# Kernel optimization log

Hardware: AMD Instinct MI355X
Metric: run time of the kernel (lower is better)

The kernel has to match this reference:

```python
import jax, jax.numpy as jnp
import numpy as np

M, K, O = 8192, 4096, 4096
WORDS = K // 32
INT32_MAX = 2147483647


def _unpack_ternary(nz, sgn):
    """Unpack bit-packed ternary weights.
    nz, sgn: [O, WORDS] int32 bitmasks. Bit j of word w corresponds to input
    column w*32 + j. weight = 0 if nz bit clear, else +1 (sgn bit clear) or -1.
    Returns dense float32 [O, K].
    """
    shifts = jnp.arange(32, dtype=jnp.uint32)
    nzb = (nz.astype(jnp.uint32)[:, :, None] >> shifts) & jnp.uint32(1)   # [O, WORDS, 32]
    sgb = (sgn.astype(jnp.uint32)[:, :, None] >> shifts) & jnp.uint32(1)  # [O, WORDS, 32]
    w = nzb.astype(jnp.float32) * (1.0 - 2.0 * sgb.astype(jnp.float32))
    return w.reshape(nz.shape[0], -1)  # [O, K]


def setup_inputs() -> dict:
    key = jax.random.key(0)
    k1, k2, k3, k4, k5 = jax.random.split(key, 5)
    x = jax.random.normal(k1, (M, K), dtype=jnp.float32)
    nz = jax.random.randint(k2, (O, WORDS), 0, INT32_MAX, dtype=jnp.int32)
    sgn = jax.random.randint(k3, (O, WORDS), 0, INT32_MAX, dtype=jnp.int32)
    bias = jax.random.normal(k4, (O,), dtype=jnp.float32) * 0.01
    alpha = jax.random.uniform(k5, (O,), dtype=jnp.float32, minval=0.5, maxval=1.5)
    return {"x": x, "nz": nz, "sgn": sgn, "bias": bias, "alpha": alpha}


def reference(x, nz, sgn, bias, alpha):
    # y = (x @ W^T) * alpha + bias, W dequantized from ternary bit-packs
    W = _unpack_ternary(nz, sgn)                       # [O, K]
    y = jnp.einsum('mk,ok->mo', x, W)                  # [M, O]
    y = y * alpha[None, :] + bias[None, :]
    return y
```

## Files before the change

kernel.cpp:

```cpp
#include <hip/hip_runtime.h>
#include <stdint.h>

#define M_DIM 8192
#define K_DIM 4096
#define O_DIM 4096
#define NWORDS 128

typedef __attribute__((ext_vector_type(8))) short bf16x8;
typedef __attribute__((ext_vector_type(4))) float f32x4;
typedef __attribute__((ext_vector_type(4))) float fvec4;
typedef __attribute__((ext_vector_type(4))) unsigned uvec4;

__device__ __forceinline__ unsigned f32_to_bf16u(float f) {
  union { float f; unsigned u; } v; v.f = f;
  return (v.u + 0x7FFFu + ((v.u >> 16) & 1u)) >> 16;
}

__device__ __forceinline__ unsigned pack_bf16x2(float lo, float hi) {
  return f32_to_bf16u(lo) | (f32_to_bf16u(hi) << 16);
}

__global__ __launch_bounds__(256) void prep_kernel(const fvec4* __restrict__ x,
                                                   uvec4* __restrict__ xb4,
                                                   const unsigned* __restrict__ nz,
                                                   const unsigned* __restrict__ sgn,
                                                   unsigned short* __restrict__ wb) {
  const int b   = blockIdx.x;
  const int tid = threadIdx.x;
  if (b < 2048) {
    for (long p = (long)b * 256 + tid; p < 4194304; p += 524288) {
      const fvec4 v0 = x[2 * p];
      const fvec4 v1 = x[2 * p + 1];
      uvec4 o;
      o.x = pack_bf16x2(v0.x, v0.y);
      o.y = pack_bf16x2(v0.z, v0.w);
      o.z = pack_bf16x2(v1.x, v1.y);
      o.w = pack_bf16x2(v1.z, v1.w);
      xb4[p] = o;
    }
  } else {
    for (long i = (long)(b - 2048) * 256 + tid; i < 2097152; i += 131072) {
      const int w = (int)(i >> 2);
      const int q = (int)(i & 3);
      const unsigned n = nz[w] >> (8 * q);
      const unsigned s = sgn[w] >> (8 * q);
      unsigned out[4];
#pragma unroll
      for (int pq = 0; pq < 4; ++pq) {
        const int j0 = 2 * pq, j1 = 2 * pq + 1;
        unsigned lo = ((n >> j0) & 1u) ? (0x3F80u | (((s >> j0) & 1u) << 15)) : 0u;
        unsigned hi = ((n >> j1) & 1u) ? (0x3F80u | (((s >> j1) & 1u) << 15)) : 0u;
        out[pq] = lo | (hi << 16);
      }
      uvec4 v = { out[0], out[1], out[2], out[3] };
      *(uvec4*)(wb + (long)w * 32 + q * 8) = v;
    }
  }
}

__global__ __launch_bounds__(512, 2) void gemm_kernel(const unsigned short* __restrict__ A,
                                                      const unsigned short* __restrict__ B,
                                                      const float* __restrict__ bias,
                                                      const float* __restrict__ alpha,
                                                      float* __restrict__ C) {
  __shared__ unsigned short lds[65536];

  const int tid  = threadIdx.x;
  const int lane = tid & 63;
  const int wave = tid >> 6;
  const int wm   = wave >> 2;
  const int wn   = wave & 3;

  const int wg   = blockIdx.x;
  const int swz  = (wg & 7) * 64 + (wg >> 3);
  const int nBlk = (swz & 15) * 256;
  const int mBlk = (swz >> 4) * 256;

  const unsigned short* Apan = A + (long)mBlk * K_DIM;
  const unsigned short* Bpan = B + (long)nBlk * K_DIM;

  int lOff[2], gOff[2];
#pragma unroll
  for (int l = 0; l < 2; ++l) {
    const int o = (l * 512 + tid) * 16;
    const int r = o >> 7;
    const int q = ((o >> 4) & 7) ^ (r & 7);
    lOff[l] = o;
    gOff[l] = r * K_DIM + q * 8;
  }

  const int fr  = lane & 15;
  const int fq  = lane >> 4;
  const int sl0 = fq ^ (fr & 7);
  const int aFB = fr * 64;
  const int bFB = (wn & 1) * 4096 + fr * 64;
  const int A0S = wm * 8192;
  const int A1S = (2 + wm) * 8192;
  const int B0S = 32768 + (wn >> 1) * 8192;
  const int B1S = 32768 + (2 + (wn >> 1)) * 8192;

  f32x4  acc[8][4] = {};
  bf16x8 a[2][2], bv[4][2];

#define STAGE(SUBv, BUFv, TILEv) do {                                          \
    const unsigned short* s_ = (((SUBv) < 2) ? Apan : Bpan)                    \
        + (long)((SUBv) & 1) * (128 * K_DIM) + (long)(TILEv) * 64;             \
    const int dB = ((((SUBv) < 2) ? 0 : 32768)                                 \
        + (((BUFv) * 2) + ((SUBv) & 1)) * 8192) * 2;                           \
    __builtin_amdgcn_global_load_lds(                                          \
        (const __attribute__((address_space(1))) void*)(s_ + gOff[0]),         \
        (__attribute__((address_space(3))) void*)((char*)lds + dB + lOff[0]),  \
        16, 0, 0);                                                             \
    __builtin_amdgcn_global_load_lds(                                          \
        (const __attribute__((address_space(1))) void*)(s_ + gOff[1]),         \
        (__attribute__((address_space(3))) void*)((char*)lds + dB + lOff[1]),  \
        16, 0, 0);                                                             \
  } while (0)

#define LOADA2(BASE, P)                                                        \
  _Pragma("unroll")                                                            \
  for (int i = 0; i < 2; ++i) {                                                \
    const int off_ = (BASE) + ((P) * 2 + i) * 1024 + aFB;                      \
    a[i][0] = *(const bf16x8*)(lds + off_ + sl0 * 8);                          \
    a[i][1] = *(const bf16x8*)(lds + off_ + (sl0 ^ 4) * 8);                    \
  }

#define LOADB(BASE)                                                            \
  _Pragma("unroll")                                                            \
  for (int j = 0; j < 4; ++j) {                                                \
    const int off_ = (BASE) + bFB + j * 1024;                                  \
    bv[j][0] = *(const bf16x8*)(lds + off_ + sl0 * 8);                         \
    bv[j][1] = *(const bf16x8*)(lds + off_ + (sl0 ^ 4) * 8);                   \
  }

#define MFMA2(P)                                                               \
  _Pragma("unroll")                                                            \
  for (int kh = 0; kh < 2; ++kh)                                               \
    _Pragma("unroll")                                                          \
    for (int i = 0; i < 2; ++i)                                                \
      _Pragma("unroll")                                                        \
      for (int tn = 0; tn < 4; ++tn)                                           \
        acc[(P) * 2 + i][tn] = __builtin_amdgcn_mfma_f32_16x16x32_bf16(        \
            a[i][kh], bv[tn][kh], acc[(P) * 2 + i][tn], 0, 0, 0);

#define PRE12()   asm volatile("s_waitcnt lgkmcnt(8)" ::: "memory")
#define MID()  __builtin_amdgcn_s_barrier();                                   \
               asm volatile("s_waitcnt lgkmcnt(0)" ::: "memory");              \
               __builtin_amdgcn_s_setprio(1)
#define ENDPH()   __builtin_amdgcn_s_setprio(0); __builtin_amdgcn_s_barrier()
#define ENDVM4()  __builtin_amdgcn_s_setprio(0);                               \
                  asm volatile("s_waitcnt vmcnt(4)" ::: "memory");             \
                  __builtin_amdgcn_s_barrier()
#define ENDVM0()  __builtin_amdgcn_s_setprio(0);                               \
                  asm volatile("s_waitcnt vmcnt(0)" ::: "memory");             \
                  __builtin_amdgcn_s_barrier()

  STAGE(2, 0, 0); STAGE(3, 0, 0); STAGE(0, 0, 0); STAGE(1, 0, 0);
  STAGE(2, 1, 1); STAGE(3, 1, 1);
  asm volatile("s_waitcnt vmcnt(4)" ::: "memory");
  __builtin_amdgcn_s_barrier();

  for (int it = 0; it < (K_DIM / 64) / 2 - 1; ++it) {
    const int t1 = 2 * it + 1, t2 = 2 * it + 2, t3 = 2 * it + 3;
    LOADA2(A0S, 0); LOADB(B0S); STAGE(1, 1, t1); PRE12();
                                                 MID(); MFMA2(0); ENDPH();
    LOADA2(A0S, 1);             STAGE(0, 1, t1); MID(); MFMA2(1); ENDPH();
    LOADA2(A0S, 2);             STAGE(2, 0, t2); MID(); MFMA2(2); ENDPH();
    LOADA2(A0S, 3);             STAGE(3, 0, t2); MID(); MFMA2(3); ENDVM4();
    LOADA2(A1S, 0); LOADB(B1S); STAGE(0, 0, t2); PRE12();
                                                 MID(); MFMA2(0); ENDPH();
    LOADA2(A1S, 1);             STAGE(1, 0, t2); MID(); MFMA2(1); ENDPH();
    LOADA2(A1S, 2);             STAGE(2, 1, t3); MID(); MFMA2(2); ENDPH();
    LOADA2(A1S, 3);             STAGE(3, 1, t3); MID(); MFMA2(3); ENDVM4();
  }

  LOADA2(A0S, 0); LOADB(B0S); STAGE(1, 1, 63); PRE12();
                                               MID(); MFMA2(0); ENDPH();
  LOADA2(A0S, 1);             STAGE(0, 1, 63); MID(); MFMA2(1); ENDPH();
  LOADA2(A0S, 2);                              MID(); MFMA2(2); ENDPH();
  LOADA2(A0S, 3);                              MID(); MFMA2(3); ENDVM0();
  LOADA2(A1S, 0); LOADB(B1S);                  MID(); MFMA2(0); ENDPH();
  LOADA2(A1S, 1);                              MID(); MFMA2(1); ENDPH();
  LOADA2(A1S, 2);                              MID(); MFMA2(2); ENDPH();
  LOADA2(A1S, 3);                              MID(); MFMA2(3);
  __builtin_amdgcn_s_setprio(0);

#pragma unroll
  for (int tn = 0; tn < 4; ++tn) {
    const int n = nBlk + wn * 64 + tn * 16 + fr;
    const float al = alpha[n];
    const float bi = bias[n];
#pragma unroll
    for (int tm = 0; tm < 8; ++tm) {
      const int mBase = mBlk + wm * 128 + tm * 16 + fq * 4;
#pragma unroll
      for (int r = 0; r < 4; ++r)
        __builtin_nontemporal_store(acc[tm][tn][r] * al + bi,
                                    C + (long)(mBase + r) * O_DIM + n);
    }
  }

#undef STAGE
#undef LOADA2
#undef LOADB
#undef MFMA2
#undef PRE12
#undef MID
#undef ENDPH
#undef ENDVM4
#undef ENDVM0
}

__global__ __launch_bounds__(256) void fallback_kernel(const float* __restrict__ x,
                                                       const unsigned* __restrict__ nz,
                                                       const unsigned* __restrict__ sgn,
                                                       const float* __restrict__ bias,
                                                       const float* __restrict__ alpha,
                                                       float* __restrict__ y) {
  long gid = (long)blockIdx.x * 256 + threadIdx.x;
  int o = (int)(gid % O_DIM);
  long m = gid / O_DIM;
  const float* xr = x + m * K_DIM;
  float s = 0.f;
  for (int w = 0; w < NWORDS; ++w) {
    unsigned n = nz[o * NWORDS + w];
    unsigned g = sgn[o * NWORDS + w];
    for (int j = 0; j < 32; ++j) {
      if ((n >> j) & 1u) {
        float v = xr[w * 32 + j];
        s += ((g >> j) & 1u) ? -v : v;
      }
    }
  }
  y[gid] = s * alpha[o] + bias[o];
}

extern "C" void kernel_launch(void* const* d_in, const int* in_sizes, int n_in,
                              void* d_out, int out_size, void* d_ws, size_t ws_size,
                              hipStream_t stream) {
  const float*    x     = (const float*)d_in[0];
  const unsigned* nz    = (const unsigned*)d_in[1];
  const unsigned* sgn   = (const unsigned*)d_in[2];
  const float*    bias  = (const float*)d_in[3];
  const float*    alpha = (const float*)d_in[4];
  float*          y     = (float*)d_out;

  const size_t xb_bytes = (size_t)M_DIM * K_DIM * 2;
  const size_t wb_bytes = (size_t)O_DIM * K_DIM * 2;

  if (ws_size >= xb_bytes + wb_bytes) {
    unsigned short* xb = (unsigned short*)d_ws;
    unsigned short* wb = (unsigned short*)((char*)d_ws + xb_bytes);

    prep_kernel<<<2560, 256, 0, stream>>>((const fvec4*)x, (uvec4*)xb, nz, sgn, wb);
    gemm_kernel<<<512, 512, 0, stream>>>(xb, wb, bias, alpha, y);
  } else {
    fallback_kernel<<<(long)M_DIM * O_DIM / 256, 256, 0, stream>>>(x, nz, sgn, bias, alpha, y);
  }
}
```

Before: 435.3 us.

## Switch GEMM inner loop from 16x16x32 to 32x32x16 bf16 MFMA tiles

Replaces the 16x16x32 bf16 MFMA fragments with 32x32x16 MFMA, changing each wave's accumulator layout to 4x2 tiles of 32x32, and reworks LDS fragment loads and the epilogue store mapping to match. Larger MFMA tiles cut the LDS reads per FLOP and the MFMA instruction count. In exchange the LDS access pattern under the existing XOR swizzle changes, which may cause bank conflicts. The output index mapping must match the 32x32 accumulator layout exactly.

After: 456.6 us. +4.9%, slower.

```diff
diff --git a/kernel.cpp b/kernel.cpp
--- a/kernel.cpp
+++ b/kernel.cpp
@@ -7,7 +7,7 @@
 #define NWORDS 128
 
 typedef __attribute__((ext_vector_type(8))) short bf16x8;
-typedef __attribute__((ext_vector_type(4))) float f32x4;
+typedef __attribute__((ext_vector_type(16))) float f32x16;
 typedef __attribute__((ext_vector_type(4))) float fvec4;
 typedef __attribute__((ext_vector_type(4))) unsigned uvec4;
 
@@ -89,18 +89,21 @@
     gOff[l] = r * K_DIM + q * 8;
   }
 
-  const int fr  = lane & 15;
-  const int fq  = lane >> 4;
-  const int sl0 = fq ^ (fr & 7);
-  const int aFB = fr * 64;
-  const int bFB = (wn & 1) * 4096 + fr * 64;
+  const int rl = lane & 31;
+  const int hi = lane >> 5;
+  const int x7 = lane & 7;
+  int qs[4];
+#pragma unroll
+  for (int g = 0; g < 4; ++g) qs[g] = (2 * g + hi) ^ x7;
+  const int aRB = rl * 64;
+  const int bNB = (wn & 1) * 4096 + rl * 64;
   const int A0S = wm * 8192;
   const int A1S = (2 + wm) * 8192;
   const int B0S = 32768 + (wn >> 1) * 8192;
   const int B1S = 32768 + (2 + (wn >> 1)) * 8192;
 
-  f32x4  acc[8][4] = {};
-  bf16x8 a[2][2], bv[4][2];
+  f32x16 acc[4][2] = {};
+  bf16x8 a[4], bv[2][4];
 
 #define STAGE(SUBv, BUFv, TILEv) do {                                          \
     const unsigned short* s_ = (((SUBv) < 2) ? Apan : Bpan)                    \
@@ -117,31 +120,25 @@
         16, 0, 0);                                                             \
   } while (0)
 
-#define LOADA2(BASE, P)                                                        \
+#define LOADA32(BASE, MB)                                                      \
   _Pragma("unroll")                                                            \
-  for (int i = 0; i < 2; ++i) {                                                \
-    const int off_ = (BASE) + ((P) * 2 + i) * 1024 + aFB;                      \
-    a[i][0] = *(const bf16x8*)(lds + off_ + sl0 * 8);                          \
-    a[i][1] = *(const bf16x8*)(lds + off_ + (sl0 ^ 4) * 8);                    \
-  }
-
-#define LOADB(BASE)                                                            \
+  for (int g = 0; g < 4; ++g)                                                  \
+    a[g] = *(const bf16x8*)(lds + (BASE) + (MB) * 2048 + aRB + qs[g] * 8);
+
+#define LOADB32(BASE)                                                          \
   _Pragma("unroll")                                                            \
-  for (int j = 0; j < 4; ++j) {                                                \
-    const int off_ = (BASE) + bFB + j * 1024;                                  \
-    bv[j][0] = *(const bf16x8*)(lds + off_ + sl0 * 8);                         \
-    bv[j][1] = *(const bf16x8*)(lds + off_ + (sl0 ^ 4) * 8);                   \
-  }
-
-#define MFMA2(P)                                                               \
+  for (int nt = 0; nt < 2; ++nt)                                               \
+    _Pragma("unroll")                                                          \
+    for (int g = 0; g < 4; ++g)                                                \
+      bv[nt][g] = *(const bf16x8*)(lds + (BASE) + bNB + nt * 2048 + qs[g] * 8);
+
+#define MFMAPH(MB)                                                             \
   _Pragma("unroll")                                                            \
-  for (int kh = 0; kh < 2; ++kh)                                               \
+  for (int g = 0; g < 4; ++g)                                                  \
     _Pragma("unroll")                                                          \
-    for (int i = 0; i < 2; ++i)                                                \
-      _Pragma("unroll")                                                        \
-      for (int tn = 0; tn < 4; ++tn)                                           \
-        acc[(P) * 2 + i][tn] = __builtin_amdgcn_mfma_f32_16x16x32_bf16(        \
-            a[i][kh], bv[tn][kh], acc[(P) * 2 + i][tn], 0, 0, 0);
+    for (int nt = 0; nt < 2; ++nt)                                             \
+      acc[MB][nt] = __builtin_amdgcn_mfma_f32_32x32x16_bf16(                   \
+          a[g], bv[nt][g], acc[MB][nt], 0, 0, 0);
 
 #define PRE12()   asm volatile("s_waitcnt lgkmcnt(8)" ::: "memory")
 #define MID()  __builtin_amdgcn_s_barrier();                                   \
@@ -162,48 +159,51 @@
 
   for (int it = 0; it < (K_DIM / 64) / 2 - 1; ++it) {
     const int t1 = 2 * it + 1, t2 = 2 * it + 2, t3 = 2 * it + 3;
-    LOADA2(A0S, 0); LOADB(B0S); STAGE(1, 1, t1); PRE12();
-                                                 MID(); MFMA2(0); ENDPH();
-    LOADA2(A0S, 1);             STAGE(0, 1, t1); MID(); MFMA2(1); ENDPH();
-    LOADA2(A0S, 2);             STAGE(2, 0, t2); MID(); MFMA2(2); ENDPH();
-    LOADA2(A0S, 3);             STAGE(3, 0, t2); MID(); MFMA2(3); ENDVM4();
-    LOADA2(A1S, 0); LOADB(B1S); STAGE(0, 0, t2); PRE12();
-                                                 MID(); MFMA2(0); ENDPH();
-    LOADA2(A1S, 1);             STAGE(1, 0, t2); MID(); MFMA2(1); ENDPH();
-    LOADA2(A1S, 2);             STAGE(2, 1, t3); MID(); MFMA2(2); ENDPH();
-    LOADA2(A1S, 3);             STAGE(3, 1, t3); MID(); MFMA2(3); ENDVM4();
-  }
-
-  LOADA2(A0S, 0); LOADB(B0S); STAGE(1, 1, 63); PRE12();
-                                               MID(); MFMA2(0); ENDPH();
-  LOADA2(A0S, 1);             STAGE(0, 1, 63); MID(); MFMA2(1); ENDPH();
-  LOADA2(A0S, 2);                              MID(); MFMA2(2); ENDPH();
-  LOADA2(A0S, 3);                              MID(); MFMA2(3); ENDVM0();
-  LOADA2(A1S, 0); LOADB(B1S);                  MID(); MFMA2(0); ENDPH();
-  LOADA2(A1S, 1);                              MID(); MFMA2(1); ENDPH();
-  LOADA2(A1S, 2);                              MID(); MFMA2(2); ENDPH();
-  LOADA2(A1S, 3);                              MID(); MFMA2(3);
+    LOADA32(A0S, 0); LOADB32(B0S); STAGE(1, 1, t1); PRE12();
+                                                    MID(); MFMAPH(0); ENDPH();
+    LOADA32(A0S, 1);               STAGE(0, 1, t1); MID(); MFMAPH(1); ENDPH();
+    LOADA32(A0S, 2);               STAGE(2, 0, t2); MID(); MFMAPH(2); ENDPH();
+    LOADA32(A0S, 3);               STAGE(3, 0, t2); MID(); MFMAPH(3); ENDVM4();
+    LOADA32(A1S, 0); LOADB32(B1S); STAGE(0, 0, t2); PRE12();
+                                                    MID(); MFMAPH(0); ENDPH();
+    LOADA32(A1S, 1);               STAGE(1, 0, t2); MID(); MFMAPH(1); ENDPH();
+    LOADA32(A1S, 2);               STAGE(2, 1, t3); MID(); MFMAPH(2); ENDPH();
+    LOADA32(A1S, 3);               STAGE(3, 1, t3); MID(); MFMAPH(3); ENDVM4();
+  }
+
+  LOADA32(A0S, 0); LOADB32(B0S); STAGE(1, 1, 63); PRE12();
+                                                  MID(); MFMAPH(0); ENDPH();
+  LOADA32(A0S, 1);               STAGE(0, 1, 63); MID(); MFMAPH(1); ENDPH();
+  LOADA32(A0S, 2);                                MID(); MFMAPH(2); ENDPH();
+  LOADA32(A0S, 3);                                MID(); MFMAPH(3); ENDVM0();
+  LOADA32(A1S, 0); LOADB32(B1S);                  MID(); MFMAPH(0); ENDPH();
+  LOADA32(A1S, 1);                                MID(); MFMAPH(1); ENDPH();
+  LOADA32(A1S, 2);                                MID(); MFMAPH(2); ENDPH();
+  LOADA32(A1S, 3);                                MID(); MFMAPH(3);
   __builtin_amdgcn_s_setprio(0);
 
-#pragma unroll
-  for (int tn = 0; tn < 4; ++tn) {
-    const int n = nBlk + wn * 64 + tn * 16 + fr;
+  const int nB0 = nBlk + wn * 64;
+#pragma unroll
+  for (int nt = 0; nt < 2; ++nt) {
+    const int n = nB0 + nt * 32 + rl;
     const float al = alpha[n];
     const float bi = bias[n];
 #pragma unroll
-    for (int tm = 0; tm < 8; ++tm) {
-      const int mBase = mBlk + wm * 128 + tm * 16 + fq * 4;
-#pragma unroll
-      for (int r = 0; r < 4; ++r)
-        __builtin_nontemporal_store(acc[tm][tn][r] * al + bi,
-                                    C + (long)(mBase + r) * O_DIM + n);
+    for (int mb = 0; mb < 4; ++mb) {
+      const int mBase = mBlk + wm * 128 + mb * 32 + 4 * hi;
+#pragma unroll
+      for (int r = 0; r < 16; ++r) {
+        const int m = mBase + (r & 3) + 8 * (r >> 2);
+        __builtin_nontemporal_store(acc[mb][nt][r] * al + bi,
+                                    C + (long)m * O_DIM + n);
+      }
     }
   }
 
 #undef STAGE
-#undef LOADA2
-#undef LOADB
-#undef MFMA2
+#undef LOADA32
+#undef LOADB32
+#undef MFMAPH
 #undef PRE12
 #undef MID
 #undef ENDPH
```

## Software-pipeline LDS fragment loads one phase ahead of MFMA segments

Applied to the files above, without the earlier changes.

Restructures the main GEMM loop so each phase issues the LDS reads and global stages for the next phase right after its MFMA block, instead of before its own. The end-of-phase barrier is removed; a single barrier plus lgkmcnt(0) wait now sits at the start of each segment. The intent is to overlap LDS read latency with the preceding MFMA work and cut one barrier per phase. The risk is higher register pressure from fragments in flight and possible LDS hazards, since a barrier no longer separates reads from later stage writes.

Result: no change. 429.4 us (-1.3%).

```diff
diff --git a/kernel.cpp b/kernel.cpp
--- a/kernel.cpp
+++ b/kernel.cpp
@@ -143,46 +143,47 @@
         acc[(P) * 2 + i][tn] = __builtin_amdgcn_mfma_f32_16x16x32_bf16(        \
             a[i][kh], bv[tn][kh], acc[(P) * 2 + i][tn], 0, 0, 0);
 
-#define PRE12()   asm volatile("s_waitcnt lgkmcnt(8)" ::: "memory")
-#define MID()  __builtin_amdgcn_s_barrier();                                   \
+#define SEGH() __builtin_amdgcn_s_barrier();                                   \
                asm volatile("s_waitcnt lgkmcnt(0)" ::: "memory");              \
                __builtin_amdgcn_s_setprio(1)
-#define ENDPH()   __builtin_amdgcn_s_setprio(0); __builtin_amdgcn_s_barrier()
-#define ENDVM4()  __builtin_amdgcn_s_setprio(0);                               \
-                  asm volatile("s_waitcnt vmcnt(4)" ::: "memory");             \
-                  __builtin_amdgcn_s_barrier()
-#define ENDVM0()  __builtin_amdgcn_s_setprio(0);                               \
-                  asm volatile("s_waitcnt vmcnt(0)" ::: "memory");             \
-                  __builtin_amdgcn_s_barrier()
+#define PLO()  __builtin_amdgcn_s_setprio(0)
+#define EVM4() __builtin_amdgcn_s_setprio(0);                                  \
+               asm volatile("s_waitcnt vmcnt(4)" ::: "memory");                \
+               __builtin_amdgcn_s_barrier()
+#define EVM0() __builtin_amdgcn_s_setprio(0);                                  \
+               asm volatile("s_waitcnt vmcnt(0)" ::: "memory");                \
+               __builtin_amdgcn_s_barrier()
 
   STAGE(2, 0, 0); STAGE(3, 0, 0); STAGE(0, 0, 0); STAGE(1, 0, 0);
   STAGE(2, 1, 1); STAGE(3, 1, 1);
   asm volatile("s_waitcnt vmcnt(4)" ::: "memory");
   __builtin_amdgcn_s_barrier();
+  LOADA2(A0S, 0); LOADB(B0S);
+  STAGE(1, 1, 1);
 
   for (int it = 0; it < (K_DIM / 64) / 2 - 1; ++it) {
     const int t1 = 2 * it + 1, t2 = 2 * it + 2, t3 = 2 * it + 3;
-    LOADA2(A0S, 0); LOADB(B0S); STAGE(1, 1, t1); PRE12();
-                                                 MID(); MFMA2(0); ENDPH();
-    LOADA2(A0S, 1);             STAGE(0, 1, t1); MID(); MFMA2(1); ENDPH();
-    LOADA2(A0S, 2);             STAGE(2, 0, t2); MID(); MFMA2(2); ENDPH();
-    LOADA2(A0S, 3);             STAGE(3, 0, t2); MID(); MFMA2(3); ENDVM4();
-    LOADA2(A1S, 0); LOADB(B1S); STAGE(0, 0, t2); PRE12();
-                                                 MID(); MFMA2(0); ENDPH();
-    LOADA2(A1S, 1);             STAGE(1, 0, t2); MID(); MFMA2(1); ENDPH();
-    LOADA2(A1S, 2);             STAGE(2, 1, t3); MID(); MFMA2(2); ENDPH();
-    LOADA2(A1S, 3);             STAGE(3, 1, t3); MID(); MFMA2(3); ENDVM4();
-  }
-
-  LOADA2(A0S, 0); LOADB(B0S); STAGE(1, 1, 63); PRE12();
-                                               MID(); MFMA2(0); ENDPH();
-  LOADA2(A0S, 1);             STAGE(0, 1, 63); MID(); MFMA2(1); ENDPH();
-  LOADA2(A0S, 2);                              MID(); MFMA2(2); ENDPH();
-  LOADA2(A0S, 3);                              MID(); MFMA2(3); ENDVM0();
-  LOADA2(A1S, 0); LOADB(B1S);                  MID(); MFMA2(0); ENDPH();
-  LOADA2(A1S, 1);                              MID(); MFMA2(1); ENDPH();
-  LOADA2(A1S, 2);                              MID(); MFMA2(2); ENDPH();
-  LOADA2(A1S, 3);                              MID(); MFMA2(3);
+    SEGH(); MFMA2(0); PLO(); LOADA2(A0S, 1); STAGE(0, 1, t1);
+    SEGH(); MFMA2(1); PLO(); LOADA2(A0S, 2); STAGE(2, 0, t2);
+    SEGH(); MFMA2(2); PLO(); LOADA2(A0S, 3); STAGE(3, 0, t2);
+    SEGH(); MFMA2(3); EVM4();
+    LOADA2(A1S, 0); LOADB(B1S); STAGE(0, 0, t2);
+    SEGH(); MFMA2(0); PLO(); LOADA2(A1S, 1); STAGE(1, 0, t2);
+    SEGH(); MFMA2(1); PLO(); LOADA2(A1S, 2); STAGE(2, 1, t3);
+    SEGH(); MFMA2(2); PLO(); LOADA2(A1S, 3); STAGE(3, 1, t3);
+    SEGH(); MFMA2(3); EVM4();
+    LOADA2(A0S, 0); LOADB(B0S); STAGE(1, 1, t3);
+  }
+
+  SEGH(); MFMA2(0); PLO(); LOADA2(A0S, 1); STAGE(0, 1, 63);
+  SEGH(); MFMA2(1); PLO(); LOADA2(A0S, 2);
+  SEGH(); MFMA2(2); PLO(); LOADA2(A0S, 3);
+  SEGH(); MFMA2(3); EVM0();
+  LOADA2(A1S, 0); LOADB(B1S);
+  SEGH(); MFMA2(0); PLO(); LOADA2(A1S, 1);
+  SEGH(); MFMA2(1); PLO(); LOADA2(A1S, 2);
+  SEGH(); MFMA2(2); PLO(); LOADA2(A1S, 3);
+  SEGH(); MFMA2(3);
   __builtin_amdgcn_s_setprio(0);
 
 #pragma unroll
@@ -204,11 +205,10 @@
 #undef LOADA2
 #undef LOADB
 #undef MFMA2
-#undef PRE12
-#undef MID
-#undef ENDPH
-#undef ENDVM4
-#undef ENDVM0
+#undef SEGH
+#undef PLO
+#undef EVM4
+#undef EVM0
 }
 
 __global__ __launch_bounds__(256) void fallback_kernel(const float* __restrict__ x,
```
